# Optimization experiments

Hardware: AMD Instinct MI355X
Metric: run time of the kernel (lower is better)

## Reference

```python
import jax, jax.numpy as jnp
import numpy as np

WINDOW = (2, 7, 7)
NUM_HEADS = 4
DIM = 128


def _relative_position_index(ws):
    d, h, w = ws
    coords = np.stack(np.meshgrid(np.arange(d), np.arange(h), np.arange(w), indexing='ij'))  # (3,d,h,w)
    cf = coords.reshape(3, -1)  # (3, N)
    rel = cf[:, :, None] - cf[:, None, :]  # (3, N, N)
    rel = rel.transpose(1, 2, 0).astype(np.int64)
    rel[:, :, 0] += d - 1
    rel[:, :, 1] += h - 1
    rel[:, :, 2] += w - 1
    rel[:, :, 0] *= (2 * h - 1) * (2 * w - 1)
    rel[:, :, 1] *= 2 * w - 1
    return rel.sum(-1).astype(np.int32)  # (N, N)


def setup_inputs() -> dict:
    key = jax.random.key(0)
    ks = jax.random.split(key, 6)
    N = WINDOW[0] * WINDOW[1] * WINDOW[2]  # 98
    B_, nW, C = 4096, 64, DIM
    x = jax.random.normal(ks[0], (B_, N, C), dtype=jnp.float32)
    mask = jax.random.normal(ks[1], (nW, N, N), dtype=jnp.float32)
    qkv_w = jax.random.normal(ks[2], (3 * C, C), dtype=jnp.float32) * (C ** -0.5)
    proj_w = jax.random.normal(ks[3], (C, C), dtype=jnp.float32) * (C ** -0.5)
    proj_b = jax.random.normal(ks[4], (C,), dtype=jnp.float32) * 0.02
    n_bias = (2 * WINDOW[0] - 1) * (2 * WINDOW[1] - 1) * (2 * WINDOW[2] - 1)  # 507
    bias_table = jax.random.normal(ks[5], (n_bias, NUM_HEADS), dtype=jnp.float32) * 0.02
    rel_index = jnp.asarray(_relative_position_index(WINDOW))
    return {"x": x, "mask": mask, "qkv_w": qkv_w, "proj_w": proj_w,
            "proj_b": proj_b, "bias_table": bias_table, "rel_index": rel_index}


def reference(x, mask, qkv_w, proj_w, proj_b, bias_table, rel_index):
    B_, N, C = x.shape
    H = NUM_HEADS
    hd = C // H
    scale = hd ** -0.5
    # qkv projection (no bias), split heads -> (3, B_, H, N, hd)
    qkv = (x @ qkv_w.T).reshape(B_, N, 3, H, hd).transpose(2, 0, 3, 1, 4)
    q, k, v = qkv[0] * scale, qkv[1], qkv[2]
    attn = jnp.einsum('bhnd,bhmd->bhnm', q, k)  # (B_, H, N, N)
    # gathered relative position bias -> (H, N, N)
    bias = bias_table[rel_index.reshape(-1)].reshape(N, N, H).transpose(2, 0, 1)
    attn = attn + bias[None]
    nW = mask.shape[0]
    attn = attn.reshape(B_ // nW, nW, H, N, N) + mask[None, :, None]
    attn = jax.nn.softmax(attn.reshape(B_, H, N, N), axis=-1)
    out = jnp.einsum('bhnm,bhmd->bhnd', attn, v)  # (B_, H, N, hd)
    out = out.transpose(0, 2, 1, 3).reshape(B_, N, C)
    return out @ proj_w.T + proj_b
```

## Files before the change

### kernel.cpp

```cpp
#include <hip/hip_runtime.h>

typedef __attribute__((ext_vector_type(8))) short bf8;
typedef __attribute__((ext_vector_type(4))) float f4;
typedef __attribute__((ext_vector_type(16))) float f16v;
typedef __attribute__((ext_vector_type(2))) unsigned int u32x2;
typedef __attribute__((ext_vector_type(4))) unsigned int u32x4;

#define MFMA16(A,B,C) __builtin_amdgcn_mfma_f32_16x16x32_bf16(A,B,C,0,0,0)
#define MFMA32(A,B,C) __builtin_amdgcn_mfma_f32_32x32x16_bf16(A,B,C,0,0,0)

#define NTOK 98
#define SROW 136
#define LOG2E 1.4426950408889634f
#define QSCALE (0.17677669529663687f * LOG2E)

__device__ __forceinline__ unsigned short bfu(float f) {
  union { float f; unsigned u; } un; un.f = f;
  unsigned r = un.u + 0x7FFFu + ((un.u >> 16) & 1u);
  return (unsigned short)(r >> 16);
}
__device__ __forceinline__ unsigned cvtpk(float a, float b) {
  unsigned r;
  asm("v_cvt_pk_bf16_f32 %0, %1, %2" : "=v"(r) : "v"(a), "v"(b));
  return r;
}
__device__ __forceinline__ float h2f(unsigned short u) {
  return (float)__builtin_bit_cast(_Float16, u);
}

__global__ void prep_kernel(const float* __restrict__ qkv_w,
                            const float* __restrict__ proj_w,
                            const float* __restrict__ bias_table,
                            const int* __restrict__ rel_index,
                            const float* __restrict__ mask,
                            unsigned short* __restrict__ wq,
                            unsigned short* __restrict__ wp,
                            float* __restrict__ bsmall,
                            unsigned short* __restrict__ bmh, int use_bm) {
  const int T1 = 384*128, T2 = T1 + 128*128;
  const int TS = 4*128*112;
  const int T3 = T2 + TS;
  const int TB = 64*4*128*112;
  const int total = T3 + (use_bm ? TB : 0);
  for (int idx = blockIdx.x*blockDim.x + threadIdx.x; idx < total;
       idx += gridDim.x*blockDim.x) {
    if (idx < T1)      wq[idx] = bfu(qkv_w[idx]);
    else if (idx < T2) wp[idx - T1] = bfu(proj_w[idx - T1]);
    else if (idx < T3) {
      int t = idx - T2;
      int m = t % 112, n = (t/112) & 127, h = t / (112*128);
      float v;
      if (m >= NTOK)      v = -1e30f;
      else if (n >= NTOK) v = 0.f;
      else                v = bias_table[rel_index[n*98+m]*4 + h] * LOG2E;
      bsmall[t] = v;
    } else {
      int t = idx - T3;
      int m = t % 112; int r = t / 112;
      int n = r & 127; r >>= 7;
      int h = r & 3;   int w = r >> 2;
      float v;
      if (m >= NTOK)      v = -1e30f;
      else if (n >= NTOK) v = 0.f;
      else v = (bias_table[rel_index[n*98+m]*4 + h] + mask[(size_t)w*9604 + n*98 + m]) * LOG2E;
      bmh[t] = __builtin_bit_cast(unsigned short, (_Float16)v);
    }
  }
}

template<int USE_BM>
__launch_bounds__(1024, 1)
__global__ void wattn_kernel(const float* __restrict__ x,
                             const float* __restrict__ mask,
                             const float* __restrict__ proj_b,
                             const unsigned short* __restrict__ wqkv,
                             const unsigned short* __restrict__ wproj,
                             const float* __restrict__ bsmall,
                             const unsigned short* __restrict__ bmh,
                             float* __restrict__ out) {
  __shared__ unsigned short xb[128*SROW];
  __shared__ unsigned short qb[128*SROW];
  __shared__ unsigned short kb[128*SROW];
  __shared__ unsigned short vt[128*SROW];

  const int b = blockIdx.x, tid = threadIdx.x;
  const int wid = tid >> 6, lane = tid & 63;
  const int g = lane >> 4, c = lane & 15;
  const int hh = wid & 3, i32 = wid >> 2;
  const int l31 = lane & 31, hl = lane >> 5;
  const int n = i32*32 + l31;

  const float* xp = x + (size_t)b * (NTOK*128);
  const float4* xp4 = (const float4*)xp;
  float4 xv0 = xp4[tid];
  float4 xv1 = xp4[tid + 1024];
  float4 xv2 = xp4[tid + 2048];
  float4 xv3;
  const bool has3 = tid < 64;
  if (has3) xv3 = xp4[tid + 3072];

  ushort4 bmr[14];
  if (USE_BM) {
    const unsigned short* bp = bmh + ((size_t)((b & 63)*4 + hh)*128 + n)*112;
    #pragma unroll
    for (int j = 0; j < 3; ++j)
      #pragma unroll
      for (int a = 0; a < 4; ++a)
        bmr[j*4+a] = *(const ushort4*)(bp + j*32 + a*8 + hl*4);
    bmr[12] = *(const ushort4*)(bp + 96 + hl*4);
    bmr[13] = *(const ushort4*)(bp + 96 + 8 + hl*4);
  }

  for (int i = tid; i < 14*SROW; i += 1024) xb[98*SROW + i] = 0;
  for (int i = tid; i < 16*SROW; i += 1024) { qb[112*SROW + i] = 0; kb[112*SROW + i] = 0; }

  {
    int e = tid*4, nn = e >> 7, cc = e & 127;
    u32x2 u; u[0] = cvtpk(xv0.x, xv0.y); u[1] = cvtpk(xv0.z, xv0.w);
    *(u32x2*)&xb[nn*SROW + cc] = u;
    e = (tid+1024)*4; nn = e >> 7; cc = e & 127;
    u[0] = cvtpk(xv1.x, xv1.y); u[1] = cvtpk(xv1.z, xv1.w);
    *(u32x2*)&xb[nn*SROW + cc] = u;
    e = (tid+2048)*4; nn = e >> 7; cc = e & 127;
    u[0] = cvtpk(xv2.x, xv2.y); u[1] = cvtpk(xv2.z, xv2.w);
    *(u32x2*)&xb[nn*SROW + cc] = u;
    if (has3) {
      e = (tid+3072)*4; nn = e >> 7; cc = e & 127;
      u[0] = cvtpk(xv3.x, xv3.y); u[1] = cvtpk(xv3.z, xv3.w);
      *(u32x2*)&xb[nn*SROW + cc] = u;
    }
  }
  __syncthreads();

  for (int k3 = 0; k3 < 3; ++k3) {
    const int u = wid + 16*k3;
    const int ot = u >> 1, half = u & 1;
    const int ib = half ? 4 : 0, ni = half ? 3 : 4;
    if (ot < 16) {
      const unsigned short* wptr = wqkv + (size_t)(ot*16 + c)*128;
      f4 acc[4] = {};
      #pragma unroll
      for (int kk = 0; kk < 4; ++kk) {
        bf8 wf = *(const bf8*)(wptr + kk*32 + g*8);
        #pragma unroll
        for (int i = 0; i < 4; ++i) if (i < ni) {
          bf8 xf = *(const bf8*)(&xb[((ib+i)*16 + c)*SROW + kk*32 + g*8]);
          acc[i] = MFMA16(wf, xf, acc[i]);
        }
      }
      unsigned short* dst = (ot < 8) ? qb : kb;
      const int col = (ot & 7)*16 + g*4;
      const float sc = (ot < 8) ? QSCALE : 1.f;
      #pragma unroll
      for (int i = 0; i < 4; ++i) if (i < ni) {
        u32x2 uu;
        uu[0] = cvtpk(acc[i][0]*sc, acc[i][1]*sc);
        uu[1] = cvtpk(acc[i][2]*sc, acc[i][3]*sc);
        *(u32x2*)&dst[((ib+i)*16 + c)*SROW + col] = uu;
      }
    } else {
      const int ov = ot - 16;
      const unsigned short* wptr = wqkv + (size_t)(256 + ov*16 + c)*128;
      f4 acc[4] = {};
      #pragma unroll
      for (int kk = 0; kk < 4; ++kk) {
        bf8 wf = *(const bf8*)(wptr + kk*32 + g*8);
        #pragma unroll
        for (int i = 0; i < 4; ++i) if (i < ni) {
          bf8 xf = *(const bf8*)(&xb[((ib+i)*16 + c)*SROW + kk*32 + g*8]);
          acc[i] = MFMA16(xf, wf, acc[i]);
        }
      }
      #pragma unroll
      for (int i = 0; i < 4; ++i) if (i < ni) {
        u32x2 uu;
        uu[0] = cvtpk(acc[i][0], acc[i][1]);
        uu[1] = cvtpk(acc[i][2], acc[i][3]);
        *(u32x2*)&vt[(ov*16 + c)*SROW + (ib+i)*16 + g*4] = uu;
      }
    }
  }
  __syncthreads();

  {
    f16v sj[4];
    #pragma unroll
    for (int j = 0; j < 4; ++j)
      #pragma unroll
      for (int a = 0; a < 4; ++a) {
        if (j == 3 && a >= 2) {
          sj[j][4*a+0] = -1e30f; sj[j][4*a+1] = -1e30f;
          sj[j][4*a+2] = -1e30f; sj[j][4*a+3] = -1e30f;
        } else if (USE_BM) {
          ushort4 u = bmr[(j < 3) ? (j*4+a) : (12+a)];
          sj[j][4*a+0] = h2f(u.x); sj[j][4*a+1] = h2f(u.y);
          sj[j][4*a+2] = h2f(u.z); sj[j][4*a+3] = h2f(u.w);
        } else {
          const float* bmp = bsmall + ((size_t)hh*128 + n)*112;
          f4 t = *(const f4*)(bmp + j*32 + a*8 + hl*4);
          sj[j][4*a+0] = t[0]; sj[j][4*a+1] = t[1];
          sj[j][4*a+2] = t[2]; sj[j][4*a+3] = t[3];
        }
      }
    if (!USE_BM && n < NTOK) {
      const float* mw = mask + (size_t)(b & 63)*9604 + n*98;
      #pragma unroll
      for (int j = 0; j < 4; ++j)
        #pragma unroll
        for (int a = 0; a < 4; ++a) {
          if (j == 3 && a >= 2) continue;
          #pragma unroll
          for (int bb = 0; bb < 4; ++bb) {
            int m = j*32 + a*8 + hl*4 + bb;
            if (m < NTOK) sj[j][4*a+bb] += mw[m] * LOG2E;
          }
        }
    }
    __builtin_amdgcn_s_setprio(1);
    #pragma unroll
    for (int kd = 0; kd < 2; ++kd) {
      bf8 qf = *(const bf8*)(&qb[n*SROW + hh*32 + kd*16 + hl*8]);
      #pragma unroll
      for (int j = 0; j < 4; ++j) {
        bf8 kf = *(const bf8*)(&kb[(j*32 + l31)*SROW + hh*32 + kd*16 + hl*8]);
        sj[j] = MFMA32(kf, qf, sj[j]);
      }
    }
    __builtin_amdgcn_s_setprio(0);
    float sum = 0.f;
    #pragma unroll
    for (int j = 0; j < 4; ++j)
      #pragma unroll
      for (int r = 0; r < 16; ++r) { float e = exp2f(sj[j][r]); sj[j][r] = e; sum += e; }
    sum += __shfl_xor(sum, 32);
    const float inv = 1.f / sum;
    unsigned P2[4][4][2];
    #pragma unroll
    for (int j = 0; j < 4; ++j)
      #pragma unroll
      for (int a = 0; a < 4; ++a) {
        P2[j][a][0] = cvtpk(sj[j][4*a+0], sj[j][4*a+1]);
        P2[j][a][1] = cvtpk(sj[j][4*a+2], sj[j][4*a+3]);
      }
    f16v acc = {0.f,0.f,0.f,0.f,0.f,0.f,0.f,0.f,0.f,0.f,0.f,0.f,0.f,0.f,0.f,0.f};
    __builtin_amdgcn_s_setprio(1);
    #pragma unroll
    for (int km = 0; km < 7; ++km) {
      const int j = km >> 1, a0 = 2*(km & 1);
      bf8 vf = *(const bf8*)(&vt[(hh*32 + l31)*SROW + km*16 + hl*8]);
      unsigned o0 = P2[j][a0][0],   o1 = P2[j][a0][1];
      unsigned o2 = P2[j][a0+1][0], o3 = P2[j][a0+1][1];
      unsigned s0 = __shfl_xor(o0, 32), s1 = __shfl_xor(o1, 32);
      unsigned s2 = __shfl_xor(o2, 32), s3 = __shfl_xor(o3, 32);
      u32x4 pw;
      pw[0] = hl ? s2 : o0;  pw[1] = hl ? s3 : o1;
      pw[2] = hl ? o2 : s0;  pw[3] = hl ? o3 : s1;
      acc = MFMA32(vf, *(bf8*)&pw, acc);
    }
    __builtin_amdgcn_s_setprio(0);
    #pragma unroll
    for (int a = 0; a < 4; ++a) {
      u32x2 uu;
      uu[0] = cvtpk(acc[4*a+0]*inv, acc[4*a+1]*inv);
      uu[1] = cvtpk(acc[4*a+2]*inv, acc[4*a+3]*inv);
      *(u32x2*)&xb[n*SROW + hh*32 + a*8 + hl*4] = uu;
    }
  }
  __syncthreads();

  for (int k3 = 0; k3 < 4; ++k3) {
    const int t = wid + 16*k3;
    if (t < 56) {
      const int i = t >> 3, ot = t & 7;
      const unsigned short* wptr = wproj + (size_t)(ot*16 + c)*128;
      f4 acc = {0.f, 0.f, 0.f, 0.f};
      #pragma unroll
      for (int kk = 0; kk < 4; ++kk) {
        bf8 wf = *(const bf8*)(wptr + kk*32 + g*8);
        bf8 xf = *(const bf8*)(&xb[(i*16 + c)*SROW + kk*32 + g*8]);
        acc = MFMA16(wf, xf, acc);
      }
      const int n2 = i*16 + c;
      if (n2 < NTOK) {
        f4 pb4 = *(const f4*)(proj_b + ot*16 + g*4);
        f4 o4 = {acc[0]+pb4[0], acc[1]+pb4[1], acc[2]+pb4[2], acc[3]+pb4[3]};
        *(f4*)(out + (size_t)b*(NTOK*128) + n2*128 + ot*16 + g*4) = o4;
      }
    }
  }
}

extern "C" void kernel_launch(void* const* d_in, const int* in_sizes, int n_in,
                              void* d_out, int out_size, void* d_ws, size_t ws_size,
                              hipStream_t stream) {
  const float* x          = (const float*)d_in[0];
  const float* mask       = (const float*)d_in[1];
  const float* qkv_w      = (const float*)d_in[2];
  const float* proj_w     = (const float*)d_in[3];
  const float* proj_b     = (const float*)d_in[4];
  const float* bias_table = (const float*)d_in[5];
  const int*   rel_index  = (const int*)d_in[6];

  unsigned short* wq = (unsigned short*)d_ws;
  unsigned short* wp = wq + 384*128;
  float* bsmall = (float*)((char*)d_ws + 131072);
  unsigned short* bmh = (unsigned short*)((char*)d_ws + 360448);

  const size_t need = 360448u + (size_t)64*4*128*112*2;
  const int use_bm = (ws_size >= need) ? 1 : 0;

  prep_kernel<<<2048, 256, 0, stream>>>(qkv_w, proj_w, bias_table, rel_index, mask,
                                        wq, wp, bsmall, bmh, use_bm);
  if (use_bm)
    wattn_kernel<1><<<4096, 1024, 0, stream>>>(x, mask, proj_b, wq, wp, bsmall, bmh,
                                               (float*)d_out);
  else
    wattn_kernel<0><<<4096, 1024, 0, stream>>>(x, mask, proj_b, wq, wp, bsmall, bmh,
                                               (float*)d_out);
}
```

Measured before the change: 320.0 us.

## Store combined bias+mask as fp32, load late, skip padded exp, hoist proj weights

The precomputed bias+mask table is now stored as fp32 and read right before the QK MFMA, instead of fp16 values prefetched into registers at kernel start. The exp over padded columns is skipped and those columns are zeroed directly, and the s_setprio hints are removed. The output projection now assigns each wave a fixed column tile and loads its weight fragments and bias once, reusing them across rows. In exchange the table takes twice the memory and bandwidth, and moving its load late may expose latency that the early prefetch used to hide.

```diff
diff --git a/kernel.cpp b/kernel.cpp
--- a/kernel.cpp
+++ b/kernel.cpp
@@ -23,9 +23,6 @@
   unsigned r;
   asm("v_cvt_pk_bf16_f32 %0, %1, %2" : "=v"(r) : "v"(a), "v"(b));
   return r;
-}
-__device__ __forceinline__ float h2f(unsigned short u) {
-  return (float)__builtin_bit_cast(_Float16, u);
 }
 
 __global__ void prep_kernel(const float* __restrict__ qkv_w,
@@ -36,7 +33,7 @@
                             unsigned short* __restrict__ wq,
                             unsigned short* __restrict__ wp,
                             float* __restrict__ bsmall,
-                            unsigned short* __restrict__ bmh, int use_bm) {
+                            float* __restrict__ bmf, int use_bm) {
   const int T1 = 384*128, T2 = T1 + 128*128;
   const int TS = 4*128*112;
   const int T3 = T2 + TS;
@@ -63,7 +60,7 @@
       if (m >= NTOK)      v = -1e30f;
       else if (n >= NTOK) v = 0.f;
       else v = (bias_table[rel_index[n*98+m]*4 + h] + mask[(size_t)w*9604 + n*98 + m]) * LOG2E;
-      bmh[t] = __builtin_bit_cast(unsigned short, (_Float16)v);
+      bmf[t] = v;
     }
   }
 }
@@ -76,7 +73,7 @@
                              const unsigned short* __restrict__ wqkv,
                              const unsigned short* __restrict__ wproj,
                              const float* __restrict__ bsmall,
-                             const unsigned short* __restrict__ bmh,
+                             const float* __restrict__ bmf,
                              float* __restrict__ out) {
   __shared__ unsigned short xb[128*SROW];
   __shared__ unsigned short qb[128*SROW];
@@ -88,28 +85,15 @@
   const int g = lane >> 4, c = lane & 15;
   const int hh = wid & 3, i32 = wid >> 2;
   const int l31 = lane & 31, hl = lane >> 5;
-  const int n = i32*32 + l31;
-
-  const float* xp = x + (size_t)b * (NTOK*128);
-  const float4* xp4 = (const float4*)xp;
+  const int nA = i32*32 + l31;
+
+  const float4* xp4 = (const float4*)(x + (size_t)b * (NTOK*128));
   float4 xv0 = xp4[tid];
   float4 xv1 = xp4[tid + 1024];
   float4 xv2 = xp4[tid + 2048];
   float4 xv3;
   const bool has3 = tid < 64;
   if (has3) xv3 = xp4[tid + 3072];
-
-  ushort4 bmr[14];
-  if (USE_BM) {
-    const unsigned short* bp = bmh + ((size_t)((b & 63)*4 + hh)*128 + n)*112;
-    #pragma unroll
-    for (int j = 0; j < 3; ++j)
-      #pragma unroll
-      for (int a = 0; a < 4; ++a)
-        bmr[j*4+a] = *(const ushort4*)(bp + j*32 + a*8 + hl*4);
-    bmr[12] = *(const ushort4*)(bp + 96 + hl*4);
-    bmr[13] = *(const ushort4*)(bp + 96 + 8 + hl*4);
-  }
 
   for (int i = tid; i < 14*SROW; i += 1024) xb[98*SROW + i] = 0;
   for (int i = tid; i < 16*SROW; i += 1024) { qb[112*SROW + i] = 0; kb[112*SROW + i] = 0; }
@@ -184,26 +168,23 @@
 
   {
     f16v sj[4];
+    const float* bmp = USE_BM ? (bmf + ((size_t)((b & 63)*4 + hh)*128 + nA)*112)
+                              : (bsmall + ((size_t)hh*128 + nA)*112);
     #pragma unroll
     for (int j = 0; j < 4; ++j)
       #pragma unroll
       for (int a = 0; a < 4; ++a) {
         if (j == 3 && a >= 2) {
-          sj[j][4*a+0] = -1e30f; sj[j][4*a+1] = -1e30f;
-          sj[j][4*a+2] = -1e30f; sj[j][4*a+3] = -1e30f;
-        } else if (USE_BM) {
-          ushort4 u = bmr[(j < 3) ? (j*4+a) : (12+a)];
-          sj[j][4*a+0] = h2f(u.x); sj[j][4*a+1] = h2f(u.y);
-          sj[j][4*a+2] = h2f(u.z); sj[j][4*a+3] = h2f(u.w);
+          sj[j][4*a+0] = 0.f; sj[j][4*a+1] = 0.f;
+          sj[j][4*a+2] = 0.f; sj[j][4*a+3] = 0.f;
         } else {
-          const float* bmp = bsmall + ((size_t)hh*128 + n)*112;
           f4 t = *(const f4*)(bmp + j*32 + a*8 + hl*4);
           sj[j][4*a+0] = t[0]; sj[j][4*a+1] = t[1];
           sj[j][4*a+2] = t[2]; sj[j][4*a+3] = t[3];
         }
       }
-    if (!USE_BM && n < NTOK) {
-      const float* mw = mask + (size_t)(b & 63)*9604 + n*98;
+    if (!USE_BM && nA < NTOK) {
+      const float* mw = mask + (size_t)(b & 63)*9604 + (size_t)nA*98;
       #pragma unroll
       for (int j = 0; j < 4; ++j)
         #pragma unroll
@@ -216,22 +197,33 @@
           }
         }
     }
-    __builtin_amdgcn_s_setprio(1);
     #pragma unroll
     for (int kd = 0; kd < 2; ++kd) {
-      bf8 qf = *(const bf8*)(&qb[n*SROW + hh*32 + kd*16 + hl*8]);
+      bf8 qf = *(const bf8*)&qb[nA*SROW + hh*32 + kd*16 + hl*8];
       #pragma unroll
       for (int j = 0; j < 4; ++j) {
-        bf8 kf = *(const bf8*)(&kb[(j*32 + l31)*SROW + hh*32 + kd*16 + hl*8]);
+        bf8 kf = *(const bf8*)&kb[(j*32 + l31)*SROW + hh*32 + kd*16 + hl*8];
         sj[j] = MFMA32(kf, qf, sj[j]);
       }
     }
-    __builtin_amdgcn_s_setprio(0);
     float sum = 0.f;
     #pragma unroll
     for (int j = 0; j < 4; ++j)
       #pragma unroll
-      for (int r = 0; r < 16; ++r) { float e = exp2f(sj[j][r]); sj[j][r] = e; sum += e; }
+      for (int a = 0; a < 4; ++a) {
+        if (j == 3 && a >= 2) {
+          sj[j][4*a+0] = 0.f; sj[j][4*a+1] = 0.f;
+          sj[j][4*a+2] = 0.f; sj[j][4*a+3] = 0.f;
+          continue;
+        }
+        float e0 = exp2f(sj[j][4*a+0]);
+        float e1 = exp2f(sj[j][4*a+1]);
+        float e2 = exp2f(sj[j][4*a+2]);
+        float e3 = exp2f(sj[j][4*a+3]);
+        sj[j][4*a+0] = e0; sj[j][4*a+1] = e1;
+        sj[j][4*a+2] = e2; sj[j][4*a+3] = e3;
+        sum += (e0 + e1) + (e2 + e3);
+      }
     sum += __shfl_xor(sum, 32);
     const float inv = 1.f / sum;
     unsigned P2[4][4][2];
@@ -242,12 +234,12 @@
         P2[j][a][0] = cvtpk(sj[j][4*a+0], sj[j][4*a+1]);
         P2[j][a][1] = cvtpk(sj[j][4*a+2], sj[j][4*a+3]);
       }
-    f16v acc = {0.f,0.f,0.f,0.f,0.f,0.f,0.f,0.f,0.f,0.f,0.f,0.f,0.f,0.f,0.f,0.f};
-    __builtin_amdgcn_s_setprio(1);
+    const f16v z16 = {0.f,0.f,0.f,0.f,0.f,0.f,0.f,0.f,0.f,0.f,0.f,0.f,0.f,0.f,0.f,0.f};
+    f16v acc = z16;
     #pragma unroll
     for (int km = 0; km < 7; ++km) {
       const int j = km >> 1, a0 = 2*(km & 1);
-      bf8 vf = *(const bf8*)(&vt[(hh*32 + l31)*SROW + km*16 + hl*8]);
+      bf8 vf = *(const bf8*)&vt[(hh*32 + l31)*SROW + km*16 + hl*8];
       unsigned o0 = P2[j][a0][0],   o1 = P2[j][a0][1];
       unsigned o2 = P2[j][a0+1][0], o3 = P2[j][a0+1][1];
       unsigned s0 = __shfl_xor(o0, 32), s1 = __shfl_xor(o1, 32);
@@ -257,32 +249,36 @@
       pw[2] = hl ? o2 : s0;  pw[3] = hl ? o3 : s1;
       acc = MFMA32(vf, *(bf8*)&pw, acc);
     }
-    __builtin_amdgcn_s_setprio(0);
     #pragma unroll
     for (int a = 0; a < 4; ++a) {
       u32x2 uu;
       uu[0] = cvtpk(acc[4*a+0]*inv, acc[4*a+1]*inv);
       uu[1] = cvtpk(acc[4*a+2]*inv, acc[4*a+3]*inv);
-      *(u32x2*)&xb[n*SROW + hh*32 + a*8 + hl*4] = uu;
+      *(u32x2*)&xb[nA*SROW + hh*32 + a*8 + hl*4] = uu;
     }
   }
   __syncthreads();
 
-  for (int k3 = 0; k3 < 4; ++k3) {
-    const int t = wid + 16*k3;
-    if (t < 56) {
-      const int i = t >> 3, ot = t & 7;
-      const unsigned short* wptr = wproj + (size_t)(ot*16 + c)*128;
+  {
+    const int ot = wid & 7;
+    const int ibase = (wid < 8) ? 0 : 4;
+    const int nrows = (wid < 8) ? 4 : 3;
+    const unsigned short* wptr = wproj + (size_t)(ot*16 + c)*128;
+    bf8 wf[4];
+    #pragma unroll
+    for (int kk = 0; kk < 4; ++kk) wf[kk] = *(const bf8*)(wptr + kk*32 + g*8);
+    f4 pb4 = *(const f4*)(proj_b + ot*16 + g*4);
+    #pragma unroll
+    for (int i = 0; i < 4; ++i) if (i < nrows) {
+      const int row = ibase + i;
       f4 acc = {0.f, 0.f, 0.f, 0.f};
       #pragma unroll
       for (int kk = 0; kk < 4; ++kk) {
-        bf8 wf = *(const bf8*)(wptr + kk*32 + g*8);
-        bf8 xf = *(const bf8*)(&xb[(i*16 + c)*SROW + kk*32 + g*8]);
-        acc = MFMA16(wf, xf, acc);
-      }
-      const int n2 = i*16 + c;
+        bf8 xf = *(const bf8*)(&xb[(row*16 + c)*SROW + kk*32 + g*8]);
+        acc = MFMA16(wf[kk], xf, acc);
+      }
+      const int n2 = row*16 + c;
       if (n2 < NTOK) {
-        f4 pb4 = *(const f4*)(proj_b + ot*16 + g*4);
         f4 o4 = {acc[0]+pb4[0], acc[1]+pb4[1], acc[2]+pb4[2], acc[3]+pb4[3]};
         *(f4*)(out + (size_t)b*(NTOK*128) + n2*128 + ot*16 + g*4) = o4;
       }
@@ -304,17 +300,17 @@
   unsigned short* wq = (unsigned short*)d_ws;
   unsigned short* wp = wq + 384*128;
   float* bsmall = (float*)((char*)d_ws + 131072);
-  unsigned short* bmh = (unsigned short*)((char*)d_ws + 360448);
-
-  const size_t need = 360448u + (size_t)64*4*128*112*2;
+  float* bmf    = (float*)((char*)d_ws + 360448);
+
+  const size_t need = 360448u + (size_t)64*4*128*112*4;
   const int use_bm = (ws_size >= need) ? 1 : 0;
 
   prep_kernel<<<2048, 256, 0, stream>>>(qkv_w, proj_w, bias_table, rel_index, mask,
-                                        wq, wp, bsmall, bmh, use_bm);
+                                        wq, wp, bsmall, bmf, use_bm);
   if (use_bm)
-    wattn_kernel<1><<<4096, 1024, 0, stream>>>(x, mask, proj_b, wq, wp, bsmall, bmh,
+    wattn_kernel<1><<<4096, 1024, 0, stream>>>(x, mask, proj_b, wq, wp, bsmall, bmf,
                                                (float*)d_out);
   else
-    wattn_kernel<0><<<4096, 1024, 0, stream>>>(x, mask, proj_b, wq, wp, bsmall, bmh,
+    wattn_kernel<0><<<4096, 1024, 0, stream>>>(x, mask, proj_b, wq, wp, bsmall, bmf,
                                                (float*)d_out);
 }
```

Measured after the change: 294.5 us. -8.0%, faster.
